# Optimization experiments

Hardware: AMD Instinct MI355X
Metric: run time of the kernel (lower is better)

Reference implementation:

```python
import jax, jax.numpy as jnp
import numpy as np

N_NODES = 50000


def _gcn_norm(edge_index, edge_weight, num_nodes):
    """Add self-loops (weight 1) and compute symmetric GCN normalization.
    Returns (src, dst, norm) over the augmented edge set."""
    src = jnp.concatenate([edge_index[0], jnp.arange(num_nodes, dtype=edge_index.dtype)])
    dst = jnp.concatenate([edge_index[1], jnp.arange(num_nodes, dtype=edge_index.dtype)])
    w = jnp.concatenate([edge_weight, jnp.ones((num_nodes,), dtype=edge_weight.dtype)])
    deg = jax.ops.segment_sum(w, dst, num_segments=num_nodes)  # [N]
    deg_inv_sqrt = jnp.where(deg > 0, jax.lax.rsqrt(jnp.where(deg > 0, deg, 1.0)), 0.0)
    norm = deg_inv_sqrt[src] * w * deg_inv_sqrt[dst]  # [E+N]
    return src, dst, norm


def _gcn_conv(x, W, b, src, dst, norm, num_nodes):
    h = x @ W                                   # [N, out] linear first (PyG order)
    msg = h[src] * norm[:, None]                # [E+N, out] gather + scale
    out = jax.ops.segment_sum(msg, dst, num_segments=num_nodes)  # scatter-add
    return out + b


def setup_inputs() -> dict:
    key = jax.random.key(0)
    ks = jax.random.split(key, 9)
    N, E = N_NODES, 800000
    x = jax.random.normal(ks[0], (N, 256), dtype=jnp.float32)
    edge_index = jax.random.randint(ks[1], (2, E), 0, N, dtype=jnp.int64)
    edge_attr = jax.random.uniform(ks[2], (E,), dtype=jnp.float32)
    W1 = jax.random.normal(ks[3], (256, 128), dtype=jnp.float32) * (1.0 / np.sqrt(256))
    b1 = jnp.zeros((128,), dtype=jnp.float32)
    W2 = jax.random.normal(ks[4], (128, 128), dtype=jnp.float32) * (1.0 / np.sqrt(128))
    b2 = jnp.zeros((128,), dtype=jnp.float32)
    W3 = jax.random.normal(ks[5], (128, 128), dtype=jnp.float32) * (1.0 / np.sqrt(128))
    b3 = jnp.zeros((128,), dtype=jnp.float32)
    return {"x": x, "edge_index": edge_index, "edge_attr": edge_attr,
            "W1": W1, "b1": b1, "W2": W2, "b2": b2, "W3": W3, "b3": b3}


def reference(x, edge_index, edge_attr, W1, b1, W2, b2, W3, b3):
    N = x.shape[0]
    src, dst, norm = _gcn_norm(edge_index, edge_attr, N)
    x1 = jax.nn.relu(_gcn_conv(x, W1, b1, src, dst, norm, N))
    x2 = jax.nn.relu(_gcn_conv(x1, W2, b2, src, dst, norm, N))
    return jax.nn.relu(_gcn_conv(x2, W3, b3, src, dst, norm, N))
```

## Files before the change

### kernel.cpp

```cpp
#include <hip/hip_runtime.h>
#include <math.h>

#define F_OUT 128
#define MAXDEG 64

typedef __attribute__((ext_vector_type(8))) short short8v;
typedef __attribute__((ext_vector_type(4))) float f32x4;
typedef unsigned long long ull;

__device__ inline ushort f2bf(float x) {
    uint u = __float_as_uint(x);
    uint r = (u + 0x7FFFu + ((u >> 16) & 1u)) >> 16;
    return (ushort)r;
}
__device__ inline float bf2f(ushort h) { return __uint_as_float((uint)h << 16); }
__device__ inline uint pack2(ushort a, ushort b) { return (uint)a | ((uint)b << 16); }

__device__ inline float slot_sumw(ull s) {
    return (float)((double)(s & ((1ull << 40) - 1)) * (1.0 / 8388608.0));
}


__global__ __launch_bounds__(128) void prep_kernel(const float* __restrict__ W1,
                                                   ushort* W1th, ushort* W1tl,
                                                   ull* slot, int n) {
    int b = blockIdx.x;
    if (b < 256) {
        int idx = b * 128 + threadIdx.x;
        int k = idx >> 7, c = idx & 127;
        float x = W1[idx];
        ushort h = f2bf(x);
        ushort l = f2bf(x - bf2f(h));
        W1th[(size_t)c * 256 + k] = h;
        W1tl[(size_t)c * 256 + k] = l;
    } else {
        int i = (b - 256) * 128 + threadIdx.x;
        if (i < n) slot[i] = 0ull;
    }
}


__device__ __forceinline__ void fill_edge(const int* __restrict__ src,
                                          const int* __restrict__ dst,
                                          const float* __restrict__ w,
                                          ull* slot, int2* es, int e) {
    int s = src[e], d = dst[e];
    float wv = w[e];
    ull inc = (1ull << 40) | (ull)(uint)(wv * 8388608.0f + 0.5f);
    ull old = atomicAdd(&slot[d], inc);
    uint pos = (uint)(old >> 40);
    if (pos < MAXDEG) es[(size_t)d * MAXDEG + pos] = make_int2(s, __float_as_int(wv));
}

__global__ void coef_kernel(int2* es, const ull* __restrict__ slot, int n) {
    int i = blockIdx.x * blockDim.x + threadIdx.x;
    if (i < n * MAXDEG) {
        int d = i >> 6;
        int pos = i & (MAXDEG - 1);
        int cnt = (int)(slot[d] >> 40);
        if (pos < cnt) {
            int2 e = es[i];
            float dsrc = rsqrtf(1.0f + slot_sumw(slot[e.x]));
            es[i].y = __float_as_int(dsrc * __int_as_float(e.y));
        }
    }
}


template <int K>
__device__ __forceinline__ void gemm_body(ushort* sAh, ushort* sAl,
                                          ushort* sBh, ushort* sBl,
                                          const float* __restrict__ in,
                                          const ushort* __restrict__ Wth,
                                          const ushort* __restrict__ Wtl,
                                          ushort* __restrict__ hbf, int n, int bb) {
    const int t = threadIdx.x;
    const int lane = t & 63;
    const int wv = t >> 6;
    const int block_row = bb * 64;

    const int arow = t >> 1;
    const int ahalf = t & 1;
    const int bcol = t;

    const int l15 = lane & 15;
    const int koct = lane >> 4;

    f32x4 acc[4][4];
    #pragma unroll
    for (int r = 0; r < 4; ++r)
        #pragma unroll
        for (int c = 0; c < 4; ++c) acc[r][c] = (f32x4){0.f, 0.f, 0.f, 0.f};

    const int grow_a = block_row + arow;
    const bool arow_ok = grow_a < n;

    for (int kt = 0; kt < K / 32; ++kt) {
        const int k0 = kt * 32;

        {
            float v[16];
            if (arow_ok) {
                const float4* p = reinterpret_cast<const float4*>(
                    &in[(size_t)grow_a * K + k0 + ahalf * 16]);
                float4 f0 = p[0], f1 = p[1], f2 = p[2], f3 = p[3];
                v[0]=f0.x; v[1]=f0.y; v[2]=f0.z; v[3]=f0.w;
                v[4]=f1.x; v[5]=f1.y; v[6]=f1.z; v[7]=f1.w;
                v[8]=f2.x; v[9]=f2.y; v[10]=f2.z; v[11]=f2.w;
                v[12]=f3.x; v[13]=f3.y; v[14]=f3.z; v[15]=f3.w;
            } else {
                #pragma unroll
                for (int i = 0; i < 16; ++i) v[i] = 0.f;
            }
            ushort hh[16], ll[16];
            #pragma unroll
            for (int i = 0; i < 16; ++i) {
                hh[i] = f2bf(v[i]);
                ll[i] = f2bf(v[i] - bf2f(hh[i]));
            }
            const int c0 = 2 * ahalf, c1 = 2 * ahalf + 1;
            *reinterpret_cast<uint4*>(&sAh[(c0 * 64 + arow) * 8]) =
                make_uint4(pack2(hh[0],hh[1]), pack2(hh[2],hh[3]), pack2(hh[4],hh[5]), pack2(hh[6],hh[7]));
            *reinterpret_cast<uint4*>(&sAh[(c1 * 64 + arow) * 8]) =
                make_uint4(pack2(hh[8],hh[9]), pack2(hh[10],hh[11]), pack2(hh[12],hh[13]), pack2(hh[14],hh[15]));
            *reinterpret_cast<uint4*>(&sAl[(c0 * 64 + arow) * 8]) =
                make_uint4(pack2(ll[0],ll[1]), pack2(ll[2],ll[3]), pack2(ll[4],ll[5]), pack2(ll[6],ll[7]));
            *reinterpret_cast<uint4*>(&sAl[(c1 * 64 + arow) * 8]) =
                make_uint4(pack2(ll[8],ll[9]), pack2(ll[10],ll[11]), pack2(ll[12],ll[13]), pack2(ll[14],ll[15]));
        }
        {
            const uint4* ph = reinterpret_cast<const uint4*>(&Wth[(size_t)bcol * K + k0]);
            const uint4* pl = reinterpret_cast<const uint4*>(&Wtl[(size_t)bcol * K + k0]);
            #pragma unroll
            for (int j = 0; j < 4; ++j)
                *reinterpret_cast<uint4*>(&sBh[(j * 128 + bcol) * 8]) = ph[j];
            #pragma unroll
            for (int j = 0; j < 4; ++j)
                *reinterpret_cast<uint4*>(&sBl[(j * 128 + bcol) * 8]) = pl[j];
        }
        __syncthreads();

        short8v a_h[4], a_l[4], b_h[4], b_l[4];
        #pragma unroll
        for (int r = 0; r < 4; ++r) {
            a_h[r] = *reinterpret_cast<const short8v*>(&sAh[(koct * 64 + r * 16 + l15) * 8]);
            a_l[r] = *reinterpret_cast<const short8v*>(&sAl[(koct * 64 + r * 16 + l15) * 8]);
        }
        #pragma unroll
        for (int c = 0; c < 4; ++c) {
            b_h[c] = *reinterpret_cast<const short8v*>(&sBh[(koct * 128 + wv * 64 + c * 16 + l15) * 8]);
            b_l[c] = *reinterpret_cast<const short8v*>(&sBl[(koct * 128 + wv * 64 + c * 16 + l15) * 8]);
        }
        #pragma unroll
        for (int r = 0; r < 4; ++r)
            #pragma unroll
            for (int c = 0; c < 4; ++c) {
                acc[r][c] = __builtin_amdgcn_mfma_f32_16x16x32_bf16(a_h[r], b_h[c], acc[r][c], 0, 0, 0);
                acc[r][c] = __builtin_amdgcn_mfma_f32_16x16x32_bf16(a_h[r], b_l[c], acc[r][c], 0, 0, 0);
                acc[r][c] = __builtin_amdgcn_mfma_f32_16x16x32_bf16(a_l[r], b_h[c], acc[r][c], 0, 0, 0);
            }
        __syncthreads();
    }

    #pragma unroll
    for (int r = 0; r < 4; ++r) {
        #pragma unroll
        for (int c = 0; c < 4; ++c) {
            int gcol = wv * 64 + c * 16 + l15;
            #pragma unroll
            for (int j = 0; j < 4; ++j) {
                int grow = block_row + r * 16 + koct * 4 + j;
                if (grow < n) hbf[(size_t)grow * F_OUT + gcol] = f2bf(acc[r][c][j]);
            }
        }
    }
}


template <int K>
__global__ __launch_bounds__(128) void gemm_presplit(const ushort* __restrict__ ahp,
                                                     const ushort* __restrict__ alp,
                                                     const ushort* __restrict__ Wth,
                                                     const ushort* __restrict__ Wtl,
                                                     ushort* __restrict__ hbf, int n) {
    __shared__ ushort sAh[64 * 32], sAl[64 * 32];
    __shared__ ushort sBh[128 * 32], sBl[128 * 32];

    const int t = threadIdx.x;
    const int lane = t & 63;
    const int wv = t >> 6;
    const int block_row = blockIdx.x * 64;

    const int arow = t >> 1;
    const int ahalf = t & 1;
    const int bcol = t;

    const int l15 = lane & 15;
    const int koct = lane >> 4;

    f32x4 acc[4][4];
    #pragma unroll
    for (int r = 0; r < 4; ++r)
        #pragma unroll
        for (int c = 0; c < 4; ++c) acc[r][c] = (f32x4){0.f, 0.f, 0.f, 0.f};

    const int grow_a = block_row + arow;
    const bool arow_ok = grow_a < n;
    const uint4 zero4 = make_uint4(0u, 0u, 0u, 0u);

    for (int kt = 0; kt < K / 32; ++kt) {
        const int k0 = kt * 32;
        const int c0 = 2 * ahalf, c1 = 2 * ahalf + 1;

        if (arow_ok) {
            const uint4* ph = reinterpret_cast<const uint4*>(&ahp[(size_t)grow_a * K + k0 + ahalf * 16]);
            const uint4* pl = reinterpret_cast<const uint4*>(&alp[(size_t)grow_a * K + k0 + ahalf * 16]);
            *reinterpret_cast<uint4*>(&sAh[(c0 * 64 + arow) * 8]) = ph[0];
            *reinterpret_cast<uint4*>(&sAh[(c1 * 64 + arow) * 8]) = ph[1];
            *reinterpret_cast<uint4*>(&sAl[(c0 * 64 + arow) * 8]) = pl[0];
            *reinterpret_cast<uint4*>(&sAl[(c1 * 64 + arow) * 8]) = pl[1];
        } else {
            *reinterpret_cast<uint4*>(&sAh[(c0 * 64 + arow) * 8]) = zero4;
            *reinterpret_cast<uint4*>(&sAh[(c1 * 64 + arow) * 8]) = zero4;
            *reinterpret_cast<uint4*>(&sAl[(c0 * 64 + arow) * 8]) = zero4;
            *reinterpret_cast<uint4*>(&sAl[(c1 * 64 + arow) * 8]) = zero4;
        }
        {
            const uint4* ph = reinterpret_cast<const uint4*>(&Wth[(size_t)bcol * K + k0]);
            const uint4* pl = reinterpret_cast<const uint4*>(&Wtl[(size_t)bcol * K + k0]);
            #pragma unroll
            for (int j = 0; j < 4; ++j)
                *reinterpret_cast<uint4*>(&sBh[(j * 128 + bcol) * 8]) = ph[j];
            #pragma unroll
            for (int j = 0; j < 4; ++j)
                *reinterpret_cast<uint4*>(&sBl[(j * 128 + bcol) * 8]) = pl[j];
        }
        __syncthreads();

        short8v a_h[4], a_l[4], b_h[4], b_l[4];
        #pragma unroll
        for (int r = 0; r < 4; ++r) {
            a_h[r] = *reinterpret_cast<const short8v*>(&sAh[(koct * 64 + r * 16 + l15) * 8]);
            a_l[r] = *reinterpret_cast<const short8v*>(&sAl[(koct * 64 + r * 16 + l15) * 8]);
        }
        #pragma unroll
        for (int c = 0; c < 4; ++c) {
            b_h[c] = *reinterpret_cast<const short8v*>(&sBh[(koct * 128 + wv * 64 + c * 16 + l15) * 8]);
            b_l[c] = *reinterpret_cast<const short8v*>(&sBl[(koct * 128 + wv * 64 + c * 16 + l15) * 8]);
        }
        #pragma unroll
        for (int r = 0; r < 4; ++r)
            #pragma unroll
            for (int c = 0; c < 4; ++c) {
                acc[r][c] = __builtin_amdgcn_mfma_f32_16x16x32_bf16(a_h[r], b_h[c], acc[r][c], 0, 0, 0);
                acc[r][c] = __builtin_amdgcn_mfma_f32_16x16x32_bf16(a_h[r], b_l[c], acc[r][c], 0, 0, 0);
                acc[r][c] = __builtin_amdgcn_mfma_f32_16x16x32_bf16(a_l[r], b_h[c], acc[r][c], 0, 0, 0);
            }
        __syncthreads();
    }

    #pragma unroll
    for (int r = 0; r < 4; ++r) {
        #pragma unroll
        for (int c = 0; c < 4; ++c) {
            int gcol = wv * 64 + c * 16 + l15;
            #pragma unroll
            for (int j = 0; j < 4; ++j) {
                int grow = block_row + r * 16 + koct * 4 + j;
                if (grow < n) hbf[(size_t)grow * F_OUT + gcol] = f2bf(acc[r][c][j]);
            }
        }
    }
}


__global__ __launch_bounds__(128) void mega1_kernel(
        const float* __restrict__ x,
        const ushort* __restrict__ W1th, const ushort* __restrict__ W1tl,
        ushort* __restrict__ hbf,
        const int* __restrict__ src, const int* __restrict__ dst,
        const float* __restrict__ w, ull* slot, int2* es,
        const float* __restrict__ W2, ushort* W2th, ushort* W2tl,
        const float* __restrict__ W3, ushort* W3th, ushort* W3tl,
        int n, int E, int GB, int FB) {
    __shared__ ushort sAh[64 * 32], sAl[64 * 32];
    __shared__ ushort sBh[128 * 32], sBl[128 * 32];

    int b = blockIdx.x;
    if (b < GB) {
        gemm_body<256>(sAh, sAl, sBh, sBl, x, W1th, W1tl, hbf, n, b);
    } else if (b < GB + FB) {
        int ebase = (b - GB) * 1024 + threadIdx.x;
        #pragma unroll
        for (int q = 0; q < 8; ++q) {
            int e = ebase + q * 128;
            if (e < E) fill_edge(src, dst, w, slot, es, e);
        }
    } else {
        int wb = b - GB - FB;
        const float* W = (wb < 128) ? W2 : W3;
        ushort* Th = (wb < 128) ? W2th : W3th;
        ushort* Tl = (wb < 128) ? W2tl : W3tl;
        int idx = (wb & 127) * 128 + threadIdx.x;
        int k = idx >> 7, c = idx & 127;
        float v = W[idx];
        ushort h = f2bf(v);
        ushort l = f2bf(v - bf2f(h));
        Th[(size_t)c * 128 + k] = h;
        Tl[(size_t)c * 128 + k] = l;
    }
}


__device__ __forceinline__ void gacc(uint u, float c, float& ax, float& ay) {
    ax += c * __uint_as_float(u << 16);
    ay += c * __uint_as_float(u & 0xFFFF0000u);
}

template <bool SPLIT_OUT>
__global__ __launch_bounds__(256) void gather_kernel(const ushort* __restrict__ hbf,
                                                     const int2* __restrict__ es,
                                                     const ull* __restrict__ slot,
                                                     const float* __restrict__ bias,
                                                     ushort* __restrict__ oah,
                                                     ushort* __restrict__ oal,
                                                     float* __restrict__ outf, int n) {
    int wave = threadIdx.x >> 6;
    int lane = threadIdx.x & 63;
    int node = blockIdx.x * 4 + wave;
    if (node >= n) return;

    int f = lane * 2;
    ull sl = slot[node];
    int cnt = (int)(sl >> 40);
    if (cnt > MAXDEG) cnt = MAXDEG;
    float dd = rsqrtf(1.0f + slot_sumw(sl));

    uint hv = *reinterpret_cast<const uint*>(&hbf[(size_t)node * F_OUT + f]);
    float accx = dd * __uint_as_float(hv << 16);
    float accy = dd * __uint_as_float(hv & 0xFFFF0000u);

    const int2* ep = es + (size_t)node * MAXDEG;
    int i = 0;
    for (; i + 7 < cnt; i += 8) {
        int4 p01 = *reinterpret_cast<const int4*>(&ep[i]);
        int4 p23 = *reinterpret_cast<const int4*>(&ep[i + 2]);
        int4 p45 = *reinterpret_cast<const int4*>(&ep[i + 4]);
        int4 p67 = *reinterpret_cast<const int4*>(&ep[i + 6]);
        uint u0 = *reinterpret_cast<const uint*>(&hbf[(size_t)p01.x * F_OUT + f]);
        uint u1 = *reinterpret_cast<const uint*>(&hbf[(size_t)p01.z * F_OUT + f]);
        uint u2 = *reinterpret_cast<const uint*>(&hbf[(size_t)p23.x * F_OUT + f]);
        uint u3 = *reinterpret_cast<const uint*>(&hbf[(size_t)p23.z * F_OUT + f]);
        uint u4 = *reinterpret_cast<const uint*>(&hbf[(size_t)p45.x * F_OUT + f]);
        uint u5 = *reinterpret_cast<const uint*>(&hbf[(size_t)p45.z * F_OUT + f]);
        uint u6 = *reinterpret_cast<const uint*>(&hbf[(size_t)p67.x * F_OUT + f]);
        uint u7 = *reinterpret_cast<const uint*>(&hbf[(size_t)p67.z * F_OUT + f]);
        gacc(u0, __int_as_float(p01.y), accx, accy);
        gacc(u1, __int_as_float(p01.w), accx, accy);
        gacc(u2, __int_as_float(p23.y), accx, accy);
        gacc(u3, __int_as_float(p23.w), accx, accy);
        gacc(u4, __int_as_float(p45.y), accx, accy);
        gacc(u5, __int_as_float(p45.w), accx, accy);
        gacc(u6, __int_as_float(p67.y), accx, accy);
        gacc(u7, __int_as_float(p67.w), accx, accy);
    }
    for (; i + 1 < cnt; i += 2) {
        int4 p01 = *reinterpret_cast<const int4*>(&ep[i]);
        uint u0 = *reinterpret_cast<const uint*>(&hbf[(size_t)p01.x * F_OUT + f]);
        uint u1 = *reinterpret_cast<const uint*>(&hbf[(size_t)p01.z * F_OUT + f]);
        gacc(u0, __int_as_float(p01.y), accx, accy);
        gacc(u1, __int_as_float(p01.w), accx, accy);
    }
    if (i < cnt) {
        int2 e0 = ep[i];
        uint u0 = *reinterpret_cast<const uint*>(&hbf[(size_t)e0.x * F_OUT + f]);
        gacc(u0, __int_as_float(e0.y), accx, accy);
    }

    float rx = fmaxf(bias[f]     + dd * accx, 0.f);
    float ry = fmaxf(bias[f + 1] + dd * accy, 0.f);

    if (SPLIT_OUT) {
        ushort hx = f2bf(rx), hy = f2bf(ry);
        ushort lx = f2bf(rx - bf2f(hx)), ly = f2bf(ry - bf2f(hy));
        *reinterpret_cast<uint*>(&oah[(size_t)node * F_OUT + f]) = pack2(hx, hy);
        *reinterpret_cast<uint*>(&oal[(size_t)node * F_OUT + f]) = pack2(lx, ly);
    } else {
        *reinterpret_cast<float2*>(&outf[(size_t)node * F_OUT + f]) = make_float2(rx, ry);
    }
}


extern "C" void kernel_launch(void* const* d_in, const int* in_sizes, int n_in,
                              void* d_out, int out_size, void* d_ws, size_t ws_size,
                              hipStream_t stream) {
    const float* x  = (const float*)d_in[0];
    const int*   ei = (const int*)  d_in[1];
    const float* ew = (const float*)d_in[2];
    const float* W1 = (const float*)d_in[3];
    const float* b1 = (const float*)d_in[4];
    const float* W2 = (const float*)d_in[5];
    const float* b2 = (const float*)d_in[6];
    const float* W3 = (const float*)d_in[7];
    const float* b3 = (const float*)d_in[8];
    float* out = (float*)d_out;

    const int E = in_sizes[2];
    const int n = in_sizes[0] / 256;
    const int* src = ei;
    const int* dst = ei + E;

    char* ws = (char*)d_ws;
    ull*   slot  = (ull*)ws;
    int2*  es    = (int2*)(slot + n);
    ushort* hbf  = (ushort*)(es + (size_t)n * MAXDEG);
    ushort* aah  = hbf + (size_t)n * F_OUT;
    ushort* aal  = aah + (size_t)n * F_OUT;
    ushort* W1th = aal + (size_t)n * F_OUT;
    ushort* W1tl = W1th + 128 * 256;
    ushort* W2th = W1tl + 128 * 256;
    ushort* W2tl = W2th + 128 * 128;
    ushort* W3th = W2tl + 128 * 128;
    ushort* W3tl = W3th + 128 * 128;

    const int GB = (n + 63) / 64;
    const int FB = (E + 1023) / 1024;
    const int prep_grid = 256 + (n + 127) / 128;

    prep_kernel<<<prep_grid, 128, 0, stream>>>(W1, W1th, W1tl, slot, n);

    mega1_kernel<<<GB + FB + 256, 128, 0, stream>>>(
        x, W1th, W1tl, hbf, src, dst, ew, slot, es,
        W2, W2th, W2tl, W3, W3th, W3tl, n, E, GB, FB);

    coef_kernel<<<(n * MAXDEG + 255) / 256, 256, 0, stream>>>(es, slot, n);

    const int gather_grid = (n + 3) / 4;

    gather_kernel<true><<<gather_grid, 256, 0, stream>>>(hbf, es, slot, b1, aah, aal, nullptr, n);

    gemm_presplit<128><<<GB, 128, 0, stream>>>(aah, aal, W2th, W2tl, hbf, n);
    gather_kernel<true><<<gather_grid, 256, 0, stream>>>(hbf, es, slot, b2, aah, aal, nullptr, n);

    gemm_presplit<128><<<GB, 128, 0, stream>>>(aah, aal, W3th, W3tl, hbf, n);
    gather_kernel<false><<<gather_grid, 256, 0, stream>>>(hbf, es, slot, b3, nullptr, nullptr, out, n);
}
```

Baseline: 208.2 us.

## Fold source degree normalization into node features instead of per-edge coefficients

Drops the per-edge coef_kernel, which did a random gather of the source degree for every edge slot. The source-side rsqrt(deg) is instead applied once per node: a new scale kernel rescales the first-layer features, and the later GEMM epilogues multiply by a precomputed dis array. Per-node atomic slot counters are padded to a stride of 8 to spread atomics across cache lines. The cost is an extra bf16 rounding of the scaled features, a larger zero-init of the slot array, and a larger workspace.

```diff
diff --git a/kernel.cpp b/kernel.cpp
--- a/kernel.cpp
+++ b/kernel.cpp
@@ -3,6 +3,7 @@
 
 #define F_OUT 128
 #define MAXDEG 64
+#define SSTR 8
 
 typedef __attribute__((ext_vector_type(8))) short short8v;
 typedef __attribute__((ext_vector_type(4))) float f32x4;
@@ -35,7 +36,7 @@
         W1tl[(size_t)c * 256 + k] = l;
     } else {
         int i = (b - 256) * 128 + threadIdx.x;
-        if (i < n) slot[i] = 0ull;
+        if (i < n * SSTR) slot[i] = 0ull;
     }
 }
 
@@ -47,23 +48,29 @@
     int s = src[e], d = dst[e];
     float wv = w[e];
     ull inc = (1ull << 40) | (ull)(uint)(wv * 8388608.0f + 0.5f);
-    ull old = atomicAdd(&slot[d], inc);
+    ull old = atomicAdd(&slot[(size_t)d * SSTR], inc);
     uint pos = (uint)(old >> 40);
     if (pos < MAXDEG) es[(size_t)d * MAXDEG + pos] = make_int2(s, __float_as_int(wv));
 }
 
-__global__ void coef_kernel(int2* es, const ull* __restrict__ slot, int n) {
-    int i = blockIdx.x * blockDim.x + threadIdx.x;
-    if (i < n * MAXDEG) {
-        int d = i >> 6;
-        int pos = i & (MAXDEG - 1);
-        int cnt = (int)(slot[d] >> 40);
-        if (pos < cnt) {
-            int2 e = es[i];
-            float dsrc = rsqrtf(1.0f + slot_sumw(slot[e.x]));
-            es[i].y = __float_as_int(dsrc * __int_as_float(e.y));
-        }
-    }
+
+__global__ __launch_bounds__(256) void scale1_kernel(ushort* __restrict__ hbf,
+                                                     const ull* __restrict__ slot,
+                                                     float* __restrict__ dis, int n) {
+    int row = blockIdx.x * 16 + (threadIdx.x >> 4);
+    int ch  = threadIdx.x & 15;
+    if (row >= n) return;
+    float dd = rsqrtf(1.0f + slot_sumw(slot[(size_t)row * SSTR]));
+    if (ch == 0) dis[row] = dd;
+    uint4 v = *reinterpret_cast<uint4*>(&hbf[(size_t)row * F_OUT + ch * 8]);
+    uint r[4] = {v.x, v.y, v.z, v.w};
+    #pragma unroll
+    for (int j = 0; j < 4; ++j) {
+        float lo = __uint_as_float(r[j] << 16) * dd;
+        float hi = __uint_as_float(r[j] & 0xFFFF0000u) * dd;
+        r[j] = pack2(f2bf(lo), f2bf(hi));
+    }
+    *reinterpret_cast<uint4*>(&hbf[(size_t)row * F_OUT + ch * 8]) = make_uint4(r[0], r[1], r[2], r[3]);
 }
 
 
@@ -182,6 +189,7 @@
                                                      const ushort* __restrict__ alp,
                                                      const ushort* __restrict__ Wth,
                                                      const ushort* __restrict__ Wtl,
+                                                     const float* __restrict__ dis,
                                                      ushort* __restrict__ hbf, int n) {
     __shared__ ushort sAh[64 * 32], sAl[64 * 32];
     __shared__ ushort sBh[128 * 32], sBl[128 * 32];
@@ -267,7 +275,7 @@
             #pragma unroll
             for (int j = 0; j < 4; ++j) {
                 int grow = block_row + r * 16 + koct * 4 + j;
-                if (grow < n) hbf[(size_t)grow * F_OUT + gcol] = f2bf(acc[r][c][j]);
+                if (grow < n) hbf[(size_t)grow * F_OUT + gcol] = f2bf(acc[r][c][j] * dis[grow]);
             }
         }
     }
@@ -321,6 +329,7 @@
 __global__ __launch_bounds__(256) void gather_kernel(const ushort* __restrict__ hbf,
                                                      const int2* __restrict__ es,
                                                      const ull* __restrict__ slot,
+                                                     const float* __restrict__ dis,
                                                      const float* __restrict__ bias,
                                                      ushort* __restrict__ oah,
                                                      ushort* __restrict__ oal,
@@ -331,14 +340,13 @@
     if (node >= n) return;
 
     int f = lane * 2;
-    ull sl = slot[node];
-    int cnt = (int)(sl >> 40);
+    int cnt = (int)(slot[(size_t)node * SSTR] >> 40);
     if (cnt > MAXDEG) cnt = MAXDEG;
-    float dd = rsqrtf(1.0f + slot_sumw(sl));
+    float dd = dis[node];
 
     uint hv = *reinterpret_cast<const uint*>(&hbf[(size_t)node * F_OUT + f]);
-    float accx = dd * __uint_as_float(hv << 16);
-    float accy = dd * __uint_as_float(hv & 0xFFFF0000u);
+    float accx = __uint_as_float(hv << 16);
+    float accy = __uint_as_float(hv & 0xFFFF0000u);
 
     const int2* ep = es + (size_t)node * MAXDEG;
     int i = 0;
@@ -412,11 +420,12 @@
 
     char* ws = (char*)d_ws;
     ull*   slot  = (ull*)ws;
-    int2*  es    = (int2*)(slot + n);
+    int2*  es    = (int2*)(slot + (size_t)n * SSTR);
     ushort* hbf  = (ushort*)(es + (size_t)n * MAXDEG);
     ushort* aah  = hbf + (size_t)n * F_OUT;
     ushort* aal  = aah + (size_t)n * F_OUT;
-    ushort* W1th = aal + (size_t)n * F_OUT;
+    float* dis   = (float*)(aal + (size_t)n * F_OUT);
+    ushort* W1th = (ushort*)(dis + n);
     ushort* W1tl = W1th + 128 * 256;
     ushort* W2th = W1tl + 128 * 256;
     ushort* W2tl = W2th + 128 * 128;
@@ -425,7 +434,7 @@
 
     const int GB = (n + 63) / 64;
     const int FB = (E + 1023) / 1024;
-    const int prep_grid = 256 + (n + 127) / 128;
+    const int prep_grid = 256 + (n * SSTR + 127) / 128;
 
     prep_kernel<<<prep_grid, 128, 0, stream>>>(W1, W1th, W1tl, slot, n);
 
@@ -433,15 +442,15 @@
         x, W1th, W1tl, hbf, src, dst, ew, slot, es,
         W2, W2th, W2tl, W3, W3th, W3tl, n, E, GB, FB);
 
-    coef_kernel<<<(n * MAXDEG + 255) / 256, 256, 0, stream>>>(es, slot, n);
+    scale1_kernel<<<(n + 15) / 16, 256, 0, stream>>>(hbf, slot, dis, n);
 
     const int gather_grid = (n + 3) / 4;
 
-    gather_kernel<true><<<gather_grid, 256, 0, stream>>>(hbf, es, slot, b1, aah, aal, nullptr, n);
-
-    gemm_presplit<128><<<GB, 128, 0, stream>>>(aah, aal, W2th, W2tl, hbf, n);
-    gather_kernel<true><<<gather_grid, 256, 0, stream>>>(hbf, es, slot, b2, aah, aal, nullptr, n);
-
-    gemm_presplit<128><<<GB, 128, 0, stream>>>(aah, aal, W3th, W3tl, hbf, n);
-    gather_kernel<false><<<gather_grid, 256, 0, stream>>>(hbf, es, slot, b3, nullptr, nullptr, out, n);
-}
+    gather_kernel<true><<<gather_grid, 256, 0, stream>>>(hbf, es, slot, dis, b1, aah, aal, nullptr, n);
+
+    gemm_presplit<128><<<GB, 128, 0, stream>>>(aah, aal, W2th, W2tl, dis, hbf, n);
+    gather_kernel<true><<<gather_grid, 256, 0, stream>>>(hbf, es, slot, dis, b2, aah, aal, nullptr, n);
+
+    gemm_presplit<128><<<GB, 128, 0, stream>>>(aah, aal, W3th, W3tl, dis, hbf, n);
+    gather_kernel<false><<<gather_grid, 256, 0, stream>>>(hbf, es, slot, dis, b3, nullptr, nullptr, out, n);
+}
```

Result: slower. 219.0 us (+5.2%).
